# Optimization experiments

Hardware: AMD Instinct MI355X
Metric: run time of the kernel (lower is better)

## Reference

```python
import jax, jax.numpy as jnp
import numpy as np

H = 768
NH = 12
HD = H // NH  # 64


def setup_inputs() -> dict:
    key = jax.random.key(0)
    ks = jax.random.split(key, 12)
    B, SQ, SK = 8, 1024, 1024
    s = 1.0 / np.sqrt(H)
    return {
        "hidden_states": jax.random.normal(ks[0], (B, SQ, H), jnp.float32),
        "condition_embeddings": jax.random.normal(ks[1], (B, SK, H), jnp.float32),
        "condition_mask": jnp.ones((B, SK), jnp.float32),
        "Wq": jax.random.normal(ks[2], (H, H), jnp.float32) * s,
        "bq": jnp.zeros((H,), jnp.float32),
        "Wk": jax.random.normal(ks[3], (H, H), jnp.float32) * s,
        "bk": jnp.zeros((H,), jnp.float32),
        "Wv": jax.random.normal(ks[4], (H, H), jnp.float32) * s,
        "bv": jnp.zeros((H,), jnp.float32),
        "Wo": jax.random.normal(ks[5], (H, H), jnp.float32) * s,
        "bo": jnp.zeros((H,), jnp.float32),
        "ln_g": jnp.ones((H,), jnp.float32),
        "ln_b": jnp.zeros((H,), jnp.float32),
    }


def _heads(x):
    # [B, S, H] -> [B, NH, S, HD]
    B, S, _ = x.shape
    return x.reshape(B, S, NH, HD).transpose(0, 2, 1, 3)


def reference(hidden_states, condition_embeddings, condition_mask,
              Wq, bq, Wk, bk, Wv, bv, Wo, bo, ln_g, ln_b):
    q = _heads(hidden_states @ Wq.T + bq)            # [B,NH,SQ,HD]
    k = _heads(condition_embeddings @ Wk.T + bk)     # [B,NH,SK,HD]
    v = _heads(condition_embeddings @ Wv.T + bv)     # [B,NH,SK,HD]

    scores = jnp.einsum("bhqd,bhkd->bhqk", q, k) / np.sqrt(HD)
    ext_mask = (1.0 - condition_mask)[:, None, None, :] * -10000.0
    scores = scores + ext_mask
    probs = jax.nn.softmax(scores, axis=-1)          # dropout = identity (eval)

    ctx = jnp.einsum("bhqk,bhkd->bhqd", probs, v)    # [B,NH,SQ,HD]
    B, _, SQ, _ = ctx.shape
    ctx = ctx.transpose(0, 2, 1, 3).reshape(B, SQ, H)

    out = ctx @ Wo.T + bo
    x = hidden_states + out
    mu = jnp.mean(x, axis=-1, keepdims=True)
    var = jnp.var(x, axis=-1, keepdims=True)
    return (x - mu) / jnp.sqrt(var + 1e-5) * ln_g + ln_b
```

## Files before the change

### kernel.cpp

```cpp
#include <hip/hip_runtime.h>
#include <stdint.h>

#define B_ 8
#define S_ 1024
#define H_ 768
#define NH_ 12
#define HD_ 64
#define M_ (B_*S_)

typedef __attribute__((ext_vector_type(8))) short short8;
typedef __attribute__((ext_vector_type(8))) ushort ushort8;
typedef __attribute__((ext_vector_type(4))) float floatx4;

#define MFMA16(a,b,c) __builtin_amdgcn_mfma_f32_16x16x32_bf16((a),(b),(c),0,0,0)

__device__ __forceinline__ ushort f2bf(float x){
    union { float f; unsigned u; } v; v.f = x;
    unsigned r = (v.u + 0x7fffu + ((v.u >> 16) & 1u)) >> 16;
    return (ushort)r;
}

__device__ __forceinline__ void async16(const ushort* g, ushort* l){
    __builtin_amdgcn_global_load_lds(
        (const __attribute__((address_space(1))) unsigned int*)g,
        (__attribute__((address_space(3))) unsigned int*)l, 16, 0, 0);
}

__global__ __launch_bounds__(256, 8) void cvt_all(
    const float* __restrict__ hs, const float* __restrict__ ce,
    const float* __restrict__ wq, const float* __restrict__ wk,
    const float* __restrict__ wv, const float* __restrict__ wo,
    ushort* __restrict__ hsb, ushort* __restrict__ ceb,
    ushort* __restrict__ wqb, ushort* __restrict__ wkb,
    ushort* __restrict__ wvb, ushort* __restrict__ wob)
{
    const int NA = M_*H_/8;
    const int NW = H_*H_/8;
    int i = blockIdx.x*256 + threadIdx.x;
    if (i >= 2*NA + 4*NW) return;
    const float* s; ushort* d; int off;
    if (i < NA)            { s = hs; d = hsb; off = i; }
    else if (i < 2*NA)     { s = ce; d = ceb; off = i - NA; }
    else {
        int j = i - 2*NA;
        int wsel = j / NW;
        off = j - wsel*NW;
        s = (wsel==0) ? wq : (wsel==1) ? wk : (wsel==2) ? wv : wo;
        d = (wsel==0) ? wqb : (wsel==1) ? wkb : (wsel==2) ? wvb : wob;
    }
    float4 f0 = ((const float4*)s)[2*off];
    float4 f1 = ((const float4*)s)[2*off + 1];
    ushort8 u;
    u[0] = f2bf(f0.x); u[1] = f2bf(f0.y); u[2] = f2bf(f0.z); u[3] = f2bf(f0.w);
    u[4] = f2bf(f1.x); u[5] = f2bf(f1.y); u[6] = f2bf(f1.z); u[7] = f2bf(f1.w);
    ((ushort8*)d)[off] = u;
}

template<int BN, int MODE>
__device__ __forceinline__ void gemm_body(
    const ushort* __restrict__ A, const ushort* __restrict__ Bw,
    const float* __restrict__ bias, ushort* __restrict__ obf,
    float* __restrict__ of32, const float* __restrict__ resid,
    int bx, int by)
{
    constexpr int NT = BN/32;
    __shared__ ushort smem[8192 + BN*64];
    ushort* lA = smem;
    ushort* lB = smem + 8192;
    const int K = H_;
    int tid  = threadIdx.x;
    int lane = tid & 63, wave = tid >> 6;
    int m0 = bx * 128, n0 = by * BN;
    int wm = (wave >> 1) * 64, wn = (wave & 1) * (BN/2);
    int fr = lane & 15, quad = lane >> 4, quad4 = quad*4;

    floatx4 acc[4][NT];
    #pragma unroll
    for (int mt=0;mt<4;mt++)
        #pragma unroll
        for (int nt=0;nt<NT;nt++)
            acc[mt][nt] = (floatx4){0.f,0.f,0.f,0.f};

    int row0 = tid >> 3;
    int csw  = ((tid & 7) ^ (row0 & 7)) * 8;
    const ushort* Ap[4]; const ushort* Bp[NT];
    ushort* ldA_[4]; ushort* ldB_[NT];
    #pragma unroll
    for (int j=0;j<4;j++){
        int row = row0 + 32*j;
        Ap[j] = A  + (size_t)(m0 + row) * K + csw;
        ldA_[j] = lA + (tid + 256*j)*8;
    }
    #pragma unroll
    for (int j=0;j<NT;j++){
        int row = row0 + 32*j;
        Bp[j] = Bw + (size_t)(n0 + row) * K + csw;
        ldB_[j] = lB + (tid + 256*j)*8;
    }

    for (int k0 = 0; k0 < K; k0 += 64){
        #pragma unroll
        for (int j=0;j<4;j++) async16(Ap[j] + k0, ldA_[j]);
        #pragma unroll
        for (int j=0;j<NT;j++) async16(Bp[j] + k0, ldB_[j]);
        __syncthreads();
        #pragma unroll
        for (int kk=0; kk<2; kk++){
            short8 af[4], bfr[NT];
            #pragma unroll
            for (int t=0;t<4;t++){
                int ra = wm + t*16 + fr;
                af[t]  = *(const short8*)&lA[ra*64 + (((kk*4+quad) ^ (ra&7))<<3)];
            }
            #pragma unroll
            for (int t=0;t<NT;t++){
                int rb = wn + t*16 + fr;
                bfr[t] = *(const short8*)&lB[rb*64 + (((kk*4+quad) ^ (rb&7))<<3)];
            }
            #pragma unroll
            for (int mt=0;mt<4;mt++)
                #pragma unroll
                for (int nt=0;nt<NT;nt++)
                    acc[mt][nt] = MFMA16(af[mt], bfr[nt], acc[mt][nt]);
        }
        __syncthreads();
    }

    float bv_[NT];
    #pragma unroll
    for (int nt=0;nt<NT;nt++) bv_[nt] = bias[n0 + wn + nt*16 + fr];

    if constexpr (MODE == 0){
        #pragma unroll
        for (int mt=0;mt<4;mt++){
            int rb = m0 + wm + mt*16 + quad4;
            #pragma unroll
            for (int nt=0;nt<NT;nt++){
                int col = n0 + wn + nt*16 + fr;
                #pragma unroll
                for (int r=0;r<4;r++)
                    obf[(size_t)(rb + r)*H_ + col] = f2bf(acc[mt][nt][r] + bv_[nt]);
            }
        }
    } else if constexpr (MODE == 1){
        int bb = m0 >> 10, q0 = m0 & 1023;
        #pragma unroll
        for (int mt=0;mt<4;mt++){
            int ql = wm + mt*16 + quad4;
            #pragma unroll
            for (int nt=0;nt<NT;nt++){
                int dl = wn + nt*16 + fr;
                ushort4 u;
                u.x = f2bf(acc[mt][nt][0] + bv_[nt]);
                u.y = f2bf(acc[mt][nt][1] + bv_[nt]);
                u.z = f2bf(acc[mt][nt][2] + bv_[nt]);
                u.w = f2bf(acc[mt][nt][3] + bv_[nt]);
                *(ushort4*)&smem[dl*136 + ql] = u;
            }
        }
        __syncthreads();
        #pragma unroll
        for (int jj=0;jj<6;jj++){
            int mI = tid + 256*jj;
            int d  = mI >> 4;
            int qc = (mI & 15) * 8;
            short8 v = *(const short8*)&smem[d*136 + qc];
            int gcol = by*96 + d;
            int h = gcol >> 6, dd = gcol & 63;
            *(short8*)&obf[((size_t)((bb*NH_ + h)*HD_ + dd))*S_ + q0 + qc] = v;
        }
    } else {
        #pragma unroll
        for (int mt=0;mt<4;mt++){
            int rb = m0 + wm + mt*16 + quad4;
            #pragma unroll
            for (int nt=0;nt<NT;nt++){
                int col = n0 + wn + nt*16 + fr;
                #pragma unroll
                for (int r=0;r<4;r++){
                    size_t idx = (size_t)(rb + r)*H_ + col;
                    of32[idx] = acc[mt][nt][r] + bv_[nt] + resid[idx];
                }
            }
        }
    }
}

__global__ __launch_bounds__(256, 3) void gemm_qkv(
    const ushort* __restrict__ hsb, const ushort* __restrict__ ceb,
    const ushort* __restrict__ wqb, const ushort* __restrict__ wkb,
    const ushort* __restrict__ wvb,
    const float* __restrict__ bq, const float* __restrict__ bk,
    const float* __restrict__ bv,
    ushort* __restrict__ Qb, ushort* __restrict__ Kb, ushort* __restrict__ Vtb)
{
    int z = blockIdx.z;
    const ushort* A  = (z==0) ? hsb : ceb;
    const ushort* Bw = (z==0) ? wqb : (z==1) ? wkb : wvb;
    const float* bias = (z==0) ? bq : (z==1) ? bk : bv;
    if (z == 2)
        gemm_body<96,1>(A, Bw, bias, Vtb, nullptr, nullptr, blockIdx.x, blockIdx.y);
    else
        gemm_body<96,0>(A, Bw, bias, (z==0)?Qb:Kb, nullptr, nullptr, blockIdx.x, blockIdx.y);
}

__global__ __launch_bounds__(256, 3) void gemm_o(
    const ushort* __restrict__ ctxb, const ushort* __restrict__ wob,
    const float* __restrict__ bo, const float* __restrict__ hs,
    float* __restrict__ proj)
{
    gemm_body<128,2>(ctxb, wob, bo, nullptr, proj, hs, blockIdx.x, blockIdx.y);
}

__global__ __launch_bounds__(256, 3) void attn(
    const ushort* __restrict__ Q, const ushort* __restrict__ Kc,
    const ushort* __restrict__ Vt, const float* __restrict__ mask,
    ushort* __restrict__ ctx)
{
    __shared__ ushort lK[64*64];
    __shared__ ushort lV[64*64];
    __shared__ ushort lP[4][32*72];
    __shared__ float  lmask[S_];
    __shared__ float  linv[4][32];

    const float SC = 0.125f * 1.44269504f;

    int bid = blockIdx.x;
    int qt = bid & 7;
    int h  = (bid >> 3) % NH_;
    int b  = bid / (8*NH_);

    int tid  = threadIdx.x;
    int lane = tid & 63, w = tid >> 6;
    int fr = lane & 15, quad = lane >> 4;
    int quad4 = quad*4, sw = fr & 7;

    for (int i = tid; i < S_; i += 256)
        lmask[i] = (1.0f - mask[b*S_ + i]) * -14426.95f;

    short8 qf[2][2];
    #pragma unroll
    for (int nq=0;nq<2;nq++){
        const ushort* Qp = Q + (size_t)(b*S_ + qt*128 + w*32 + nq*16 + fr)*H_ + h*HD_ + quad*8;
        qf[nq][0] = *(const short8*)(Qp);
        qf[nq][1] = *(const short8*)(Qp + 32);
    }

    floatx4 O[2][4];
    #pragma unroll
    for (int mt=0;mt<2;mt++)
        #pragma unroll
        for (int nt=0;nt<4;nt++)
            O[mt][nt] = (floatx4){0.f,0.f,0.f,0.f};
    float rs0 = 0.f, rs1 = 0.f;

    int n0 = tid,       r0 = n0 >> 3, c0 = (n0 & 7) ^ (r0 & 7);
    int n1 = 256 + tid, r1 = n1 >> 3, c1 = (n1 & 7) ^ (r1 & 7);
    const ushort* pK0 = Kc + (size_t)(b*S_ + r0)*H_ + h*HD_ + c0*8;
    const ushort* pK1 = Kc + (size_t)(b*S_ + r1)*H_ + h*HD_ + c1*8;
    const ushort* pV0 = Vt + ((size_t)(b*NH_ + h)*HD_ + r0)*S_ + c0*8;
    const ushort* pV1 = Vt + ((size_t)(b*NH_ + h)*HD_ + r1)*S_ + c1*8;
    ushort* dK0 = &lK[n0*8]; ushort* dK1 = &lK[n1*8];
    ushort* dV0 = &lV[n0*8]; ushort* dV1 = &lV[n1*8];

    ushort* lPw = &lP[w][0];

    for (int kt = 0; kt < 16; kt++){
        __syncthreads();
        async16(pK0, dK0); async16(pK1, dK1);
        async16(pV0, dV0); async16(pV1, dV1);
        pK0 += (size_t)64*H_; pK1 += (size_t)64*H_;
        pV0 += 64; pV1 += 64;
        __syncthreads();

        float4 mk4[4];
        #pragma unroll
        for (int mk=0;mk<4;mk++)
            mk4[mk] = *(const float4*)&lmask[kt*64 + mk*16 + quad4];

        short8 kf[4][2];
        #pragma unroll
        for (int mk=0;mk<4;mk++){
            int row = mk*16 + fr;
            kf[mk][0] = *(const short8*)&lK[row*64 + ((quad     ^ sw)<<3)];
            kf[mk][1] = *(const short8*)&lK[row*64 + (((4+quad) ^ sw)<<3)];
        }
        __builtin_amdgcn_s_setprio(1);
        floatx4 st[2][4];
        #pragma unroll
        for (int nq=0;nq<2;nq++)
            #pragma unroll
            for (int mk=0;mk<4;mk++){
                floatx4 a = (floatx4){0.f,0.f,0.f,0.f};
                a = MFMA16(kf[mk][0], qf[nq][0], a);
                a = MFMA16(kf[mk][1], qf[nq][1], a);
                st[nq][mk] = a;
            }
        __builtin_amdgcn_s_setprio(0);

        #pragma unroll
        for (int nq=0;nq<2;nq++){
            #pragma unroll
            for (int mk=0;mk<4;mk++){
                floatx4 s = st[nq][mk];
                #pragma unroll
                for (int r=0;r<4;r++)
                    s[r] = __builtin_amdgcn_exp2f(s[r]*SC + mk4[mk][r]);
                if (nq == 0) rs0 += (s[0]+s[1]) + (s[2]+s[3]);
                else         rs1 += (s[0]+s[1]) + (s[2]+s[3]);
                unsigned lo = __builtin_amdgcn_perm(__float_as_uint(s[1]), __float_as_uint(s[0]), 0x07060302u);
                unsigned hi = __builtin_amdgcn_perm(__float_as_uint(s[3]), __float_as_uint(s[2]), 0x07060302u);
                uint2 pk; pk.x = lo; pk.y = hi;
                *(uint2*)&lPw[(nq*16 + fr)*72 + mk*16 + quad4] = pk;
            }
        }

        short8 vf[4][2];
        #pragma unroll
        for (int nt=0;nt<4;nt++){
            int row = nt*16 + fr;
            vf[nt][0] = *(const short8*)&lV[row*64 + ((quad     ^ sw)<<3)];
            vf[nt][1] = *(const short8*)&lV[row*64 + (((4+quad) ^ sw)<<3)];
        }
        short8 pf[2][2];
        #pragma unroll
        for (int mt=0;mt<2;mt++){
            pf[mt][0] = *(const short8*)&lPw[(mt*16+fr)*72 + quad*8];
            pf[mt][1] = *(const short8*)&lPw[(mt*16+fr)*72 + 32 + quad*8];
        }
        __builtin_amdgcn_s_setprio(1);
        #pragma unroll
        for (int mt=0;mt<2;mt++)
            #pragma unroll
            for (int nt=0;nt<4;nt++){
                O[mt][nt] = MFMA16(pf[mt][0], vf[nt][0], O[mt][nt]);
                O[mt][nt] = MFMA16(pf[mt][1], vf[nt][1], O[mt][nt]);
            }
        __builtin_amdgcn_s_setprio(0);
    }

    rs0 += __shfl_xor(rs0, 16); rs0 += __shfl_xor(rs0, 32);
    rs1 += __shfl_xor(rs1, 16); rs1 += __shfl_xor(rs1, 32);
    if (lane < 16){
        linv[w][fr]      = 1.0f / rs0;
        linv[w][16 + fr] = 1.0f / rs1;
    }
    int tokbase = b*S_ + qt*128 + w*32;
    #pragma unroll
    for (int mt=0;mt<2;mt++){
        float4 iv = *(const float4*)&linv[w][mt*16 + quad4];
        #pragma unroll
        for (int nt=0;nt<4;nt++)
            #pragma unroll
            for (int r=0;r<4;r++){
                int tok = tokbase + mt*16 + quad4 + r;
                ctx[(size_t)tok*H_ + h*HD_ + nt*16 + fr] = f2bf(O[mt][nt][r] * (&iv.x)[r]);
            }
    }
}

__global__ __launch_bounds__(192, 4) void resid_ln(
    const float* __restrict__ x,
    const float* __restrict__ g, const float* __restrict__ be,
    float* __restrict__ out)
{
    int row = blockIdx.x;
    int tid = threadIdx.x;
    float4 v = ((const float4*)(x + (size_t)row*H_))[tid];
    float s  = (v.x + v.y) + (v.z + v.w);
    float s2 = (v.x*v.x + v.y*v.y) + (v.z*v.z + v.w*v.w);
    #pragma unroll
    for (int off=1; off<64; off<<=1){
        s  += __shfl_xor(s,  off);
        s2 += __shfl_xor(s2, off);
    }
    __shared__ float rs[3], rs2[3];
    if ((tid & 63) == 0){ rs[tid>>6] = s; rs2[tid>>6] = s2; }
    __syncthreads();
    s  = rs[0]+rs[1]+rs[2];
    s2 = rs2[0]+rs2[1]+rs2[2];
    float mu  = s * (1.f/H_);
    float var = s2*(1.f/H_) - mu*mu;
    float rinv = rsqrtf(var + 1e-5f);
    float4 gg = ((const float4*)g)[tid];
    float4 bb = ((const float4*)be)[tid];
    float4 o;
    o.x = (v.x-mu)*rinv*gg.x + bb.x;
    o.y = (v.y-mu)*rinv*gg.y + bb.y;
    o.z = (v.z-mu)*rinv*gg.z + bb.z;
    o.w = (v.w-mu)*rinv*gg.w + bb.w;
    ((float4*)(out + (size_t)row*H_))[tid] = o;
}

extern "C" void kernel_launch(void* const* d_in, const int* in_sizes, int n_in,
                              void* d_out, int out_size, void* d_ws, size_t ws_size,
                              hipStream_t stream)
{
    (void)in_sizes; (void)n_in; (void)out_size; (void)ws_size;
    const float* hs   = (const float*)d_in[0];
    const float* ce   = (const float*)d_in[1];
    const float* mask = (const float*)d_in[2];
    const float* Wq   = (const float*)d_in[3];
    const float* bq   = (const float*)d_in[4];
    const float* Wk   = (const float*)d_in[5];
    const float* bk   = (const float*)d_in[6];
    const float* Wv   = (const float*)d_in[7];
    const float* bv   = (const float*)d_in[8];
    const float* Wo   = (const float*)d_in[9];
    const float* bo   = (const float*)d_in[10];
    const float* lg   = (const float*)d_in[11];
    const float* lb   = (const float*)d_in[12];
    float* out = (float*)d_out;

    char* ws = (char*)d_ws;
    const size_t SZ_ACT = (size_t)M_*H_*2;
    const size_t SZ_W   = (size_t)H_*H_*2;
    ushort* hsb  = (ushort*)(ws);
    ushort* ceb  = (ushort*)(ws + SZ_ACT);
    ushort* wqb  = (ushort*)(ws + 2*SZ_ACT);
    ushort* wkb  = (ushort*)(ws + 2*SZ_ACT + 1*SZ_W);
    ushort* wvb  = (ushort*)(ws + 2*SZ_ACT + 2*SZ_W);
    ushort* wob  = (ushort*)(ws + 2*SZ_ACT + 3*SZ_W);
    ushort* Qb   = (ushort*)(ws + 2*SZ_ACT + 4*SZ_W);
    ushort* Kb   = (ushort*)(ws + 3*SZ_ACT + 4*SZ_W);
    ushort* Vtb  = (ushort*)(ws + 4*SZ_ACT + 4*SZ_W);
    ushort* ctxb = (ushort*)(ws + 5*SZ_ACT + 4*SZ_W);
    float*  proj = (float*)(ws);

    int ncvt = 2*(M_*H_/8) + 4*(H_*H_/8);
    cvt_all<<<dim3((ncvt+255)/256), dim3(256), 0, stream>>>(
        hs, ce, Wq, Wk, Wv, Wo, hsb, ceb, wqb, wkb, wvb, wob);

    gemm_qkv<<<dim3(M_/128, H_/96, 3), dim3(256), 0, stream>>>(
        hsb, ceb, wqb, wkb, wvb, bq, bk, bv, Qb, Kb, Vtb);

    attn<<<dim3(B_*NH_*8), dim3(256), 0, stream>>>(Qb, Kb, Vtb, mask, ctxb);

    gemm_o<<<dim3(M_/128, H_/128), dim3(256), 0, stream>>>(ctxb, wob, bo, hs, proj);

    resid_ln<<<dim3(M_), dim3(192), 0, stream>>>(proj, lg, lb, out);
}
```

Measured before the change: 225.8 us.

## Fuse activation fp32-to-bf16 conversion into QKV GEMM A-tile loads

The separate conversion pass over hidden_states and condition_embeddings is removed. The QKV GEMM now reads fp32 activations directly, converts them to bf16 in registers and stores them to LDS, while weights keep the async global-to-LDS path. This saves a full write and re-read of two bf16 activation buffers. The cost is that the A loads become synchronous register loads and each activation tile is re-read in fp32 by every N-tile block (8 of them), doubling those bytes. The output GEMM tile width also changes from 128 to 96, which gives more blocks.

```diff
diff --git a/kernel.cpp b/kernel.cpp
--- a/kernel.cpp
+++ b/kernel.cpp
@@ -26,28 +26,19 @@
         (__attribute__((address_space(3))) unsigned int*)l, 16, 0, 0);
 }
 
-__global__ __launch_bounds__(256, 8) void cvt_all(
-    const float* __restrict__ hs, const float* __restrict__ ce,
+__global__ __launch_bounds__(256, 8) void cvt_w(
     const float* __restrict__ wq, const float* __restrict__ wk,
     const float* __restrict__ wv, const float* __restrict__ wo,
-    ushort* __restrict__ hsb, ushort* __restrict__ ceb,
     ushort* __restrict__ wqb, ushort* __restrict__ wkb,
     ushort* __restrict__ wvb, ushort* __restrict__ wob)
 {
-    const int NA = M_*H_/8;
     const int NW = H_*H_/8;
     int i = blockIdx.x*256 + threadIdx.x;
-    if (i >= 2*NA + 4*NW) return;
-    const float* s; ushort* d; int off;
-    if (i < NA)            { s = hs; d = hsb; off = i; }
-    else if (i < 2*NA)     { s = ce; d = ceb; off = i - NA; }
-    else {
-        int j = i - 2*NA;
-        int wsel = j / NW;
-        off = j - wsel*NW;
-        s = (wsel==0) ? wq : (wsel==1) ? wk : (wsel==2) ? wv : wo;
-        d = (wsel==0) ? wqb : (wsel==1) ? wkb : (wsel==2) ? wvb : wob;
-    }
+    if (i >= 4*NW) return;
+    int wsel = i / NW;
+    int off  = i - wsel*NW;
+    const float* s = (wsel==0) ? wq : (wsel==1) ? wk : (wsel==2) ? wv : wo;
+    ushort* d      = (wsel==0) ? wqb : (wsel==1) ? wkb : (wsel==2) ? wvb : wob;
     float4 f0 = ((const float4*)s)[2*off];
     float4 f1 = ((const float4*)s)[2*off + 1];
     ushort8 u;
@@ -56,9 +47,9 @@
     ((ushort8*)d)[off] = u;
 }
 
-template<int BN, int MODE>
+template<int BN, int MODE, int AF32>
 __device__ __forceinline__ void gemm_body(
-    const ushort* __restrict__ A, const ushort* __restrict__ Bw,
+    const void* __restrict__ Avoid, const ushort* __restrict__ Bw,
     const float* __restrict__ bias, ushort* __restrict__ obf,
     float* __restrict__ of32, const float* __restrict__ resid,
     int bx, int by)
@@ -83,12 +74,15 @@
 
     int row0 = tid >> 3;
     int csw  = ((tid & 7) ^ (row0 & 7)) * 8;
-    const ushort* Ap[4]; const ushort* Bp[NT];
+    const ushort* Ab[4]; const float* Af[4]; const ushort* Bp[NT];
     ushort* ldA_[4]; ushort* ldB_[NT];
     #pragma unroll
     for (int j=0;j<4;j++){
         int row = row0 + 32*j;
-        Ap[j] = A  + (size_t)(m0 + row) * K + csw;
+        if constexpr (AF32)
+            Af[j] = (const float*)Avoid + (size_t)(m0 + row) * K + csw;
+        else
+            Ab[j] = (const ushort*)Avoid + (size_t)(m0 + row) * K + csw;
         ldA_[j] = lA + (tid + 256*j)*8;
     }
     #pragma unroll
@@ -99,8 +93,23 @@
     }
 
     for (int k0 = 0; k0 < K; k0 += 64){
-        #pragma unroll
-        for (int j=0;j<4;j++) async16(Ap[j] + k0, ldA_[j]);
+        if constexpr (AF32){
+            #pragma unroll
+            for (int j=0;j<4;j++){
+                const float* p = Af[j] + k0;
+                float4 f0 = *(const float4*)p;
+                float4 f1 = *(const float4*)(p + 4);
+                ushort8 u;
+                u[0] = f2bf(f0.x); u[1] = f2bf(f0.y);
+                u[2] = f2bf(f0.z); u[3] = f2bf(f0.w);
+                u[4] = f2bf(f1.x); u[5] = f2bf(f1.y);
+                u[6] = f2bf(f1.z); u[7] = f2bf(f1.w);
+                *(ushort8*)ldA_[j] = u;
+            }
+        } else {
+            #pragma unroll
+            for (int j=0;j<4;j++) async16(Ab[j] + k0, ldA_[j]);
+        }
         #pragma unroll
         for (int j=0;j<NT;j++) async16(Bp[j] + k0, ldB_[j]);
         __syncthreads();
@@ -187,7 +196,7 @@
 }
 
 __global__ __launch_bounds__(256, 3) void gemm_qkv(
-    const ushort* __restrict__ hsb, const ushort* __restrict__ ceb,
+    const float* __restrict__ hs, const float* __restrict__ ce,
     const ushort* __restrict__ wqb, const ushort* __restrict__ wkb,
     const ushort* __restrict__ wvb,
     const float* __restrict__ bq, const float* __restrict__ bk,
@@ -195,13 +204,13 @@
     ushort* __restrict__ Qb, ushort* __restrict__ Kb, ushort* __restrict__ Vtb)
 {
     int z = blockIdx.z;
-    const ushort* A  = (z==0) ? hsb : ceb;
+    const float* A   = (z==0) ? hs : ce;
     const ushort* Bw = (z==0) ? wqb : (z==1) ? wkb : wvb;
     const float* bias = (z==0) ? bq : (z==1) ? bk : bv;
     if (z == 2)
-        gemm_body<96,1>(A, Bw, bias, Vtb, nullptr, nullptr, blockIdx.x, blockIdx.y);
+        gemm_body<96,1,1>(A, Bw, bias, Vtb, nullptr, nullptr, blockIdx.x, blockIdx.y);
     else
-        gemm_body<96,0>(A, Bw, bias, (z==0)?Qb:Kb, nullptr, nullptr, blockIdx.x, blockIdx.y);
+        gemm_body<96,0,1>(A, Bw, bias, (z==0)?Qb:Kb, nullptr, nullptr, blockIdx.x, blockIdx.y);
 }
 
 __global__ __launch_bounds__(256, 3) void gemm_o(
@@ -209,7 +218,7 @@
     const float* __restrict__ bo, const float* __restrict__ hs,
     float* __restrict__ proj)
 {
-    gemm_body<128,2>(ctxb, wob, bo, nullptr, proj, hs, blockIdx.x, blockIdx.y);
+    gemm_body<96,2,0>(ctxb, wob, bo, nullptr, proj, hs, blockIdx.x, blockIdx.y);
 }
 
 __global__ __launch_bounds__(256, 3) void attn(
@@ -415,8 +424,6 @@
     char* ws = (char*)d_ws;
     const size_t SZ_ACT = (size_t)M_*H_*2;
     const size_t SZ_W   = (size_t)H_*H_*2;
-    ushort* hsb  = (ushort*)(ws);
-    ushort* ceb  = (ushort*)(ws + SZ_ACT);
     ushort* wqb  = (ushort*)(ws + 2*SZ_ACT);
     ushort* wkb  = (ushort*)(ws + 2*SZ_ACT + 1*SZ_W);
     ushort* wvb  = (ushort*)(ws + 2*SZ_ACT + 2*SZ_W);
@@ -427,16 +434,16 @@
     ushort* ctxb = (ushort*)(ws + 5*SZ_ACT + 4*SZ_W);
     float*  proj = (float*)(ws);
 
-    int ncvt = 2*(M_*H_/8) + 4*(H_*H_/8);
-    cvt_all<<<dim3((ncvt+255)/256), dim3(256), 0, stream>>>(
-        hs, ce, Wq, Wk, Wv, Wo, hsb, ceb, wqb, wkb, wvb, wob);
+    int ncvt = 4*(H_*H_/8);
+    cvt_w<<<dim3((ncvt+255)/256), dim3(256), 0, stream>>>(
+        Wq, Wk, Wv, Wo, wqb, wkb, wvb, wob);
 
     gemm_qkv<<<dim3(M_/128, H_/96, 3), dim3(256), 0, stream>>>(
-        hsb, ceb, wqb, wkb, wvb, bq, bk, bv, Qb, Kb, Vtb);
+        hs, ce, wqb, wkb, wvb, bq, bk, bv, Qb, Kb, Vtb);
 
     attn<<<dim3(B_*NH_*8), dim3(256), 0, stream>>>(Qb, Kb, Vtb, mask, ctxb);
 
-    gemm_o<<<dim3(M_/128, H_/128), dim3(256), 0, stream>>>(ctxb, wob, bo, hs, proj);
+    gemm_o<<<dim3(M_/128, H_/96), dim3(256), 0, stream>>>(ctxb, wob, bo, hs, proj);
 
     resid_ln<<<dim3(M_), dim3(192), 0, stream>>>(proj, lg, lb, out);
 }
```

After: 240.4 us. +6.5%, slower.
